# Performance work log

Hardware: AMD Instinct MI355X
Metric: run time of the kernel (lower is better)

## Reference

```python
import jax, jax.numpy as jnp
import numpy as np

HEADS, KV_HEADS, HEAD_DIM = 32, 8, 64


def apply_rope(x, cos, sin):
    # x: [b,h,s,d], cos/sin: [s, d//2]; pairs are interleaved (even/odd)
    c = cos[None, None, :, :]
    s = sin[None, None, :, :]
    x1 = x[..., 0::2]
    x2 = x[..., 1::2]
    xn = x1 * c - x2 * s
    yn = x1 * s + x2 * c
    return jnp.stack([xn, yn], axis=-1).reshape(x.shape)


def setup_inputs() -> dict:
    key = jax.random.key(0)
    ks = jax.random.split(key, 7)
    b, s, h = 1, 2048, 2048
    return {
        "x": jax.random.normal(ks[0], (b, s, h), jnp.float32),
        "cos": jax.random.normal(ks[1], (s, HEAD_DIM // 2), jnp.float32),
        "sin": jax.random.normal(ks[2], (s, HEAD_DIM // 2), jnp.float32),
        "Wq": jax.random.normal(ks[3], (h, HEADS * HEAD_DIM), jnp.float32) * 0.02,
        "Wk": jax.random.normal(ks[4], (h, KV_HEADS * HEAD_DIM), jnp.float32) * 0.02,
        "Wv": jax.random.normal(ks[5], (h, KV_HEADS * HEAD_DIM), jnp.float32) * 0.02,
        "Wo": jax.random.normal(ks[6], (HEADS * HEAD_DIM, h), jnp.float32) * 0.02,
    }


def reference(x, cos, sin, Wq, Wk, Wv, Wo):
    b, seq, hidden = x.shape
    Q = x @ Wq  # [b,s,H*d]
    K = x @ Wk  # [b,s,Kh*d]
    V = x @ Wv
    q = Q.reshape(b, seq, HEADS, HEAD_DIM).transpose(0, 2, 1, 3)      # b h s d
    k = K.reshape(b, seq, KV_HEADS, HEAD_DIM).transpose(0, 2, 1, 3)   # b k s d
    v = V.reshape(b, seq, KV_HEADS, HEAD_DIM).transpose(0, 2, 1, 3)
    r = HEADS // KV_HEADS
    # einops 'b k s d -> b (r k) s d': tile kv-head block r times
    k = jnp.tile(k, (1, r, 1, 1))
    v = jnp.tile(v, (1, r, 1, 1))
    q = apply_rope(q, cos, sin)
    k = apply_rope(k, cos, sin)
    scale = 1.0 / jnp.sqrt(jnp.float32(HEAD_DIM))
    qk = jnp.einsum('bhqd,bhkd->bhqk', q, k) * scale
    mask = jnp.triu(jnp.full((seq, seq), -jnp.inf, qk.dtype), k=1)
    attn = jax.nn.softmax(qk + mask, axis=-1)
    av = jnp.einsum('bhqk,bhkd->bhqd', attn, v)
    av = av.transpose(0, 2, 1, 3).reshape(b, seq, HEADS * HEAD_DIM)
    return av @ Wo
```

## Files before the change

kernel.cpp:

```cpp
#include <hip/hip_runtime.h>

typedef unsigned short u16;
typedef __attribute__((ext_vector_type(4))) float f32x4;
typedef __attribute__((ext_vector_type(16))) float f32x16;
typedef __attribute__((ext_vector_type(8))) __bf16 bf16x8;
typedef __attribute__((ext_vector_type(2))) __bf16 bf16x2;

#define HEADS 32
#define KV_HEADS 8
#define HD 64
#define SEQ 2048
#define HID 2048
#define NQK 3072
#define QSCALE (0.125f * 1.4426950408889634f)
#define OCH 2097152u

#define AS1 __attribute__((address_space(1)))
#define AS3 __attribute__((address_space(3)))

__device__ __forceinline__ u16 f2bf(float f) {
  unsigned u = __float_as_uint(f);
  u += 0x7FFFu + ((u >> 16) & 1u);
  return (u16)(u >> 16);
}

__device__ __forceinline__ unsigned pk2(float a, float b) {
  union { bf16x2 h; unsigned u; } c;
  c.h[0] = (__bf16)a; c.h[1] = (__bf16)b;
  return c.u;
}

__device__ __forceinline__ float bflo(unsigned u) {
  return __uint_as_float(u << 16);
}
__device__ __forceinline__ float bfhi(unsigned u) {
  return __uint_as_float(u & 0xFFFF0000u);
}

__device__ __forceinline__ void load16_to_lds(const void* g, void* l) {
  __builtin_amdgcn_global_load_lds((AS1 void*)(void*)g, (AS3 void*)l, 16, 0, 0);
}

__global__ __launch_bounds__(256) void k_f2b(const float* __restrict__ in,
                                             u16* __restrict__ out, int n4) {
  int i = blockIdx.x * 256 + threadIdx.x;
  if (i >= n4) return;
  float4 v = ((const float4*)in)[i];
  ushort4 o;
  o.x = f2bf(v.x); o.y = f2bf(v.y); o.z = f2bf(v.z); o.w = f2bf(v.w);
  ((ushort4*)out)[i] = o;
}

__global__ __launch_bounds__(256) void k_tconv4(const float* __restrict__ Wq,
                                                const float* __restrict__ Wk,
                                                const float* __restrict__ Wv,
                                                const float* __restrict__ Wo,
                                                u16* __restrict__ Wqkv,
                                                u16* __restrict__ WoT) {
  __shared__ float tile[32][33];
  int bid = blockIdx.x;
  const float* in; u16* out; int ldi, cx, cy;
  if (bid < 4096) {
    in = Wq; out = Wqkv; ldi = 2048; cx = bid & 63; cy = bid >> 6;
  } else if (bid < 5120) {
    int b = bid - 4096;
    in = Wk; out = Wqkv + (size_t)2048 * 2048; ldi = 512; cx = b & 15; cy = b >> 4;
  } else if (bid < 6144) {
    int b = bid - 5120;
    in = Wv; out = Wqkv + (size_t)2560 * 2048; ldi = 512; cx = b & 15; cy = b >> 4;
  } else {
    int b = bid - 6144;
    in = Wo; out = WoT; ldi = 2048; cx = b & 63; cy = b >> 6;
  }
  const int ldo = 2048;
  int c0 = cx * 32, r0 = cy * 32;
  int col = threadIdx.x & 31, rw = threadIdx.x >> 5;
#pragma unroll
  for (int i = 0; i < 4; i++)
    tile[rw + i * 8][col] = in[(size_t)(r0 + rw + i * 8) * ldi + c0 + col];
  __syncthreads();
#pragma unroll
  for (int i = 0; i < 4; i++)
    out[(size_t)(c0 + rw + i * 8) * ldo + r0 + col] = f2bf(tile[col][rw + i * 8]);
}


__device__ __forceinline__ void stage8(const u16* Ap, const u16* Bp, u16* AsX,
                                       u16* BsX, int tid, int K, int koff) {
#pragma unroll
  for (int i = 0; i < 4; i++) {
    load16_to_lds(Ap + (size_t)(i * 32) * K + koff, AsX + (i * 256 + tid) * 8);
    load16_to_lds(Bp + (size_t)(i * 32) * K + koff, BsX + (i * 256 + tid) * 8);
  }
}

__device__ __forceinline__ void frag16(const u16* Asb, const u16* Bsb,
                                       const int aoff[4][2], const int boff[4][2],
                                       f32x4 acc[4][4]) {
#pragma unroll
  for (int kk = 0; kk < 2; kk++) {
    bf16x8 a[4], b[4];
#pragma unroll
    for (int i = 0; i < 4; i++)
      a[i] = *(const bf16x8*)((const char*)Asb + aoff[i][kk]);
#pragma unroll
    for (int j = 0; j < 4; j++)
      b[j] = *(const bf16x8*)((const char*)Bsb + boff[j][kk]);
#pragma unroll
    for (int i = 0; i < 4; i++)
#pragma unroll
      for (int j = 0; j < 4; j++)
        acc[i][j] = __builtin_amdgcn_mfma_f32_16x16x32_bf16(a[i], b[j], acc[i][j], 0, 0, 0);
  }
}

#define TILE_STEP(AsX, BsX, tnext)                              \
  do {                                                          \
    asm volatile("s_waitcnt vmcnt(8)" ::: "memory");            \
    __builtin_amdgcn_sched_barrier(0);                          \
    __builtin_amdgcn_s_barrier();                               \
    frag16(AsX, BsX, aoff, boff, acc);                          \
    __builtin_amdgcn_sched_barrier(0);                          \
    __builtin_amdgcn_s_barrier();                               \
    stage8(Ap, Bp, AsX, BsX, tid, K, (tnext) * 64);             \
    __builtin_amdgcn_sched_barrier(0);                          \
  } while (0)

#define TILE_TAIL(AsX, BsX, n)                                  \
  do {                                                          \
    asm volatile("s_waitcnt vmcnt(" #n ")" ::: "memory");       \
    __builtin_amdgcn_sched_barrier(0);                          \
    __builtin_amdgcn_s_barrier();                               \
    frag16(AsX, BsX, aoff, boff, acc);                          \
  } while (0)

__global__ __launch_bounds__(256) void k_gemm(const u16* __restrict__ A,
                                              const u16* __restrict__ Bt,
                                              float* __restrict__ C,
                                              int M, int N, int K) {
  __shared__ u16 smem[32768];
  u16* As0 = smem;          u16* As1 = smem + 8192;
  u16* Bs0 = smem + 16384;  u16* Bs1 = smem + 24576;
  int tid = threadIdx.x;
  int m0 = blockIdx.x * 128, n0 = blockIdx.y * 128;
  int l = tid & 63, w = tid >> 6;
  int lr = l & 15, lg = l >> 4;
  int wr = (w >> 1) * 64, wc = (w & 1) * 64;
  f32x4 acc[4][4] = {};
  int r8 = tid >> 3;
  int sx = (tid & 7) ^ (r8 & 7);
  const u16* Ap = A + (size_t)(m0 + r8) * K + sx * 8;
  const u16* Bp = Bt + (size_t)(n0 + r8) * K + sx * 8;
  int aoff[4][2], boff[4][2];
#pragma unroll
  for (int i = 0; i < 4; i++) {
    int ra = wr + i * 16 + lr;
    int rb = wc + i * 16 + lr;
#pragma unroll
    for (int kk = 0; kk < 2; kk++) {
      aoff[i][kk] = ra * 128 + (((lg + kk * 4) ^ (ra & 7)) << 4);
      boff[i][kk] = rb * 128 + (((lg + kk * 4) ^ (rb & 7)) << 4);
    }
  }
  stage8(Ap, Bp, As0, Bs0, tid, K, 0);
  stage8(Ap, Bp, As1, Bs1, tid, K, 64);
#pragma unroll 1
  for (int t = 0; t < 30; t += 2) {
    TILE_STEP(As0, Bs0, t + 2);
    TILE_STEP(As1, Bs1, t + 3);
  }
  TILE_TAIL(As0, Bs0, 8);
  TILE_TAIL(As1, Bs1, 0);

#pragma unroll
  for (int i = 0; i < 4; i++)
#pragma unroll
    for (int j = 0; j < 4; j++)
#pragma unroll
      for (int r = 0; r < 4; r++)
        C[(size_t)(m0 + wr + i * 16 + lg * 4 + r) * N + n0 + wc + j * 16 + lr] =
            acc[i][j][r];
}


__device__ __forceinline__ void stageQ(const u16* Ap, const u16* Bp, u16* S,
                                       int tid, int koff) {
#pragma unroll
  for (int i = 0; i < 2; i++)
    load16_to_lds(Ap + (size_t)(i * 32) * HID + koff, S + (i * 256 + tid) * 8);
#pragma unroll
  for (int i = 0; i < 6; i++)
    load16_to_lds(Bp + (size_t)(i * 32) * HID + koff, S + 4096 + (i * 256 + tid) * 8);
}

__device__ __forceinline__ void frag26(const u16* Sb, const int aoff[2][2],
                                       const int boff[6][2], f32x4 acc[2][6]) {
#pragma unroll
  for (int kk = 0; kk < 2; kk++) {
    bf16x8 a[2], b[6];
#pragma unroll
    for (int i = 0; i < 2; i++)
      a[i] = *(const bf16x8*)((const char*)Sb + aoff[i][kk]);
#pragma unroll
    for (int j = 0; j < 6; j++)
      b[j] = *(const bf16x8*)((const char*)Sb + 8192 + boff[j][kk]);
    __builtin_amdgcn_s_setprio(1);
#pragma unroll
    for (int i = 0; i < 2; i++)
#pragma unroll
      for (int j = 0; j < 6; j++)
        acc[i][j] = __builtin_amdgcn_mfma_f32_16x16x32_bf16(a[i], b[j], acc[i][j], 0, 0, 0);
    __builtin_amdgcn_s_setprio(0);
  }
}

#define QK_STEP(Sc, tnext)                                      \
  do {                                                          \
    asm volatile("s_waitcnt vmcnt(8)" ::: "memory");            \
    __builtin_amdgcn_sched_barrier(0);                          \
    __builtin_amdgcn_s_barrier();                               \
    frag26(Sc, aoff, boff, acc);                                \
    __builtin_amdgcn_sched_barrier(0);                          \
    __builtin_amdgcn_s_barrier();                               \
    stageQ(Ap, Bp, Sc, tid, (tnext) * 64);                      \
    __builtin_amdgcn_sched_barrier(0);                          \
  } while (0)

#define QK_TAIL(Sc, n)                                          \
  do {                                                          \
    asm volatile("s_waitcnt vmcnt(" #n ")" ::: "memory");       \
    __builtin_amdgcn_sched_barrier(0);                          \
    __builtin_amdgcn_s_barrier();                               \
    frag26(Sc, aoff, boff, acc);                                \
  } while (0)

__global__ __launch_bounds__(256) void k_gemm_qkv(const u16* __restrict__ A,
                                                  const u16* __restrict__ Bt,
                                                  const float* __restrict__ cosp,
                                                  const float* __restrict__ sinp,
                                                  u16* __restrict__ qbuf,
                                                  u16* __restrict__ kbuf,
                                                  u16* __restrict__ vtb) {
  __shared__ u16 smem[32768];
  u16* S0 = smem;
  u16* S1 = smem + 16384;
  u16* Ts = smem;
  int tid = threadIdx.x;
  int bid = blockIdx.x;
  int wg = (bid & 7) * 64 + (bid >> 3);
  int m0 = (wg & 31) * 64, n0 = (wg >> 5) * 192;
  int l = tid & 63, w = tid >> 6;
  int lr = l & 15, lg = l >> 4;
  int wr = (w >> 1) * 32, wc = (w & 1) * 96;
  f32x4 acc[2][6] = {};
  int r8 = tid >> 3;
  int sx = (tid & 7) ^ (r8 & 7);
  const u16* Ap = A + (size_t)(m0 + r8) * HID + sx * 8;
  const u16* Bp = Bt + (size_t)(n0 + r8) * HID + sx * 8;
  int aoff[2][2], boff[6][2];
#pragma unroll
  for (int i = 0; i < 2; i++) {
    int ra = wr + i * 16 + lr;
#pragma unroll
    for (int kk = 0; kk < 2; kk++)
      aoff[i][kk] = ra * 128 + (((lg + kk * 4) ^ (ra & 7)) << 4);
  }
#pragma unroll
  for (int j = 0; j < 6; j++) {
    int rb = wc + j * 16 + lr;
#pragma unroll
    for (int kk = 0; kk < 2; kk++)
      boff[j][kk] = rb * 128 + (((lg + kk * 4) ^ (rb & 7)) << 4);
  }

  stageQ(Ap, Bp, S0, tid, 0);
  stageQ(Ap, Bp, S1, tid, 64);
#pragma unroll 1
  for (int t = 0; t < 30; t += 2) {
    QK_STEP(S0, t + 2);
    QK_STEP(S1, t + 3);
  }
  QK_TAIL(S0, 8);
  QK_TAIL(S1, 0);

  int odd = lr & 1;
#pragma unroll
  for (int j = 0; j < 6; j++) {
    int colf = n0 + wc + j * 16;
    if (colf < 2560) {
      bool isQ = colf < 2048;
      float scale = isQ ? QSCALE : 1.0f;
      u16* base = isQ ? qbuf + (size_t)(colf >> 6) * SEQ * HD
                      : kbuf + (size_t)((colf - 2048) >> 6) * SEQ * HD;
      int ch = colf & 63;
      int ii = (ch >> 1) + (lr >> 1);
#pragma unroll
      for (int i = 0; i < 2; i++)
#pragma unroll
        for (int r = 0; r < 4; r++) {
          float v = acc[i][j][r];
          float vp = __shfl_xor(v, 1, 64);
          int sr = m0 + wr + i * 16 + lg * 4 + r;
          float cs = cosp[sr * 32 + ii], sn = sinp[sr * 32 + ii];
          float x1 = odd ? vp : v, x2 = odd ? v : vp;
          float o = odd ? (x1 * sn + x2 * cs) : (x1 * cs - x2 * sn);
          base[(size_t)sr * HD + ch + lr] = f2bf(o * scale);
        }
    }
  }
  if (n0 + 192 > 2560) {
    __syncthreads();
#pragma unroll
    for (int j = 0; j < 6; j++) {
      int colf = n0 + wc + j * 16;
      if (colf >= 2560) {
#pragma unroll
        for (int i = 0; i < 2; i++)
#pragma unroll
          for (int r = 0; r < 4; r++) {
            int cB = wc + j * 16 + lr, rB = wr + i * 16 + lg * 4 + r;
            *(u16*)((char*)Ts + cB * 128 + ((rB * 2) ^ ((cB & 7) << 4))) =
                f2bf(acc[i][j][r]);
          }
      }
    }
    __syncthreads();
    int half = tid & 1;
#pragma unroll
    for (int p = 0; p < 2; p++) {
      int c = p * 128 + (tid >> 1);
      if (c < 192 && n0 + c >= 2560) {
        int col = n0 + c;
        int kvh = (col - 2560) >> 6, d = col & 63;
        u16* dst = vtb + (size_t)kvh * HD * SEQ + (size_t)d * SEQ + m0 + half * 32;
        const char* src = (const char*)Ts + c * 128;
        int cs7 = (c & 7) << 4;
#pragma unroll
        for (int q = 0; q < 4; q++)
          *(uint4*)(dst + q * 8) = *(const uint4*)(src + ((half * 64 + q * 16) ^ cs7));
      }
    }
  }
}

__global__ __launch_bounds__(256) void k_flash2(const u16* __restrict__ qb,
                                                const u16* __restrict__ kb,
                                                const u16* __restrict__ vt,
                                                unsigned* __restrict__ Opart,
                                                float2* __restrict__ ml) {
  __shared__ u16 Ks[2][64 * 64];
  __shared__ u16 Vs[2][64 * 64];
  int bid = blockIdx.x;
  int c = bid & 1;
  int b5 = bid >> 1;
  int h = b5 & 31;
  int qi = b5 >> 5;
  int qblk = (SEQ / 128) - 1 - qi;
  int kvh = h & 7;
  int tid = threadIdx.x, w = tid >> 6, l = tid & 63;
  int lq = l & 31, hi = l >> 5;
  const u16* qh = qb + (size_t)h * SEQ * HD;
  const u16* kh = kb + (size_t)kvh * SEQ * HD;
  const u16* vh = vt + (size_t)kvh * HD * SEQ;
  int wq0 = qblk * 128 + w * 32;
  int qg = wq0 + lq;

  bf16x8 qf[4];
#pragma unroll
  for (int ds = 0; ds < 4; ds++)
    qf[ds] = *(const bf16x8*)(qh + (size_t)qg * HD + ds * 16 + hi * 8);

  f32x16 acc[2] = {};
  float m_r = -__builtin_inff(), l_r = 0.f;

  int srow = tid >> 2, c4 = tid & 3, swz = (srow & 7) << 4;
  int sd0 = srow * 128 + ((c4 * 32) ^ swz);
  int sd1 = srow * 128 + ((c4 * 32 + 16) ^ swz);
  const int kt0 = c * (qblk + 1), kt1 = kt0 + qblk + 1;

  {
    const u16* ksrc = kh + (size_t)(kt0 * 64 + srow) * HD + c4 * 16;
    const u16* vsrc = vh + (size_t)srow * SEQ + kt0 * 64 + c4 * 16;
    uint4 a0 = *(const uint4*)(ksrc), a1 = *(const uint4*)(ksrc + 8);
    uint4 b0 = *(const uint4*)(vsrc), b1 = *(const uint4*)(vsrc + 8);
    *(uint4*)((char*)Ks[0] + sd0) = a0; *(uint4*)((char*)Ks[0] + sd1) = a1;
    *(uint4*)((char*)Vs[0] + sd0) = b0; *(uint4*)((char*)Vs[0] + sd1) = b1;
  }
  __syncthreads();

  uint4 kr0, kr1, vr0, vr1;
  int lswz = (lq & 7) << 4;
  for (int kt = kt0; kt < kt1; kt++) {
    int b = (kt - kt0) & 1;
    if (kt + 1 < kt1) {
      const u16* ksrc = kh + (size_t)((kt + 1) * 64 + srow) * HD + c4 * 16;
      const u16* vsrc = vh + (size_t)srow * SEQ + (kt + 1) * 64 + c4 * 16;
      kr0 = *(const uint4*)(ksrc); kr1 = *(const uint4*)(ksrc + 8);
      vr0 = *(const uint4*)(vsrc); vr1 = *(const uint4*)(vsrc + 8);
    }

    if (kt * 64 <= wq0 + 31) {
      f32x16 sT[2] = {};
      const char* kbase = (const char*)Ks[b];
      __builtin_amdgcn_s_setprio(1);
#pragma unroll
      for (int t = 0; t < 2; t++) {
#pragma unroll
        for (int ds = 0; ds < 4; ds++) {
          bf16x8 kf = *(const bf16x8*)(kbase + (t * 32 + lq) * 128 +
                                       ((ds * 32 + hi * 16) ^ lswz));
          sT[t] = __builtin_amdgcn_mfma_f32_32x32x16_bf16(kf, qf[ds], sT[t], 0, 0, 0);
        }
      }
      __builtin_amdgcn_s_setprio(0);

      if (kt * 64 + 63 > wq0) {
#pragma unroll
        for (int t = 0; t < 2; t++)
#pragma unroll
          for (int r = 0; r < 16; r++) {
            int kg = kt * 64 + t * 32 + (r & 3) + 8 * (r >> 2) + 4 * hi;
            if (kg > qg) sT[t][r] = -__builtin_inff();
          }
      }

      float pmax = sT[0][0];
#pragma unroll
      for (int r = 1; r < 16; r++) pmax = fmaxf(pmax, sT[0][r]);
#pragma unroll
      for (int r = 0; r < 16; r++) pmax = fmaxf(pmax, sT[1][r]);
      pmax = fmaxf(pmax, __shfl_xor(pmax, 32, 64));

      if (!__all(pmax <= m_r + 8.f)) {
        float mn = fmaxf(m_r, pmax);
        float scl = __builtin_amdgcn_exp2f(m_r - mn);
        l_r *= scl;
        acc[0] *= scl;
        acc[1] *= scl;
        m_r = mn;
      }

      float ss = 0.f;
#pragma unroll
      for (int t = 0; t < 2; t++)
#pragma unroll
        for (int r = 0; r < 16; r++) {
          float p = __builtin_amdgcn_exp2f(sT[t][r] - m_r);
          sT[t][r] = p;
          ss += p;
        }
      ss += __shfl_xor(ss, 32, 64);
      l_r += ss;

      const char* vbase = (const char*)Vs[b];
#pragma unroll
      for (int t = 0; t < 2; t++) {
        unsigned cp[4][2];
#pragma unroll
        for (int m = 0; m < 4; m++) {
          cp[m][0] = pk2(sT[t][4 * m + 0], sT[t][4 * m + 1]);
          cp[m][1] = pk2(sT[t][4 * m + 2], sT[t][4 * m + 3]);
        }
#pragma unroll
        for (int kl = 0; kl < 2; kl++) {
          unsigned s0 = hi ? cp[2 * kl][0] : cp[2 * kl + 1][0];
          unsigned s1 = hi ? cp[2 * kl][1] : cp[2 * kl + 1][1];
          unsigned r0 = (unsigned)__shfl_xor((int)s0, 32, 64);
          unsigned r1 = (unsigned)__shfl_xor((int)s1, 32, 64);
          union { unsigned u[4]; bf16x8 v; } pa;
          pa.u[0] = hi ? r0 : cp[2 * kl][0];
          pa.u[1] = hi ? r1 : cp[2 * kl][1];
          pa.u[2] = hi ? cp[2 * kl + 1][0] : r0;
          pa.u[3] = hi ? cp[2 * kl + 1][1] : r1;
          int ks = t * 2 + kl;
          __builtin_amdgcn_s_setprio(1);
#pragma unroll
          for (int dt = 0; dt < 2; dt++) {
            bf16x8 vb = *(const bf16x8*)(vbase + (dt * 32 + lq) * 128 +
                                         ((ks * 32 + hi * 16) ^ lswz));
            acc[dt] = __builtin_amdgcn_mfma_f32_32x32x16_bf16(vb, pa.v, acc[dt], 0, 0, 0);
          }
          __builtin_amdgcn_s_setprio(0);
        }
      }
    }

    if (kt + 1 < kt1) {
      *(uint4*)((char*)Ks[b ^ 1] + sd0) = kr0;
      *(uint4*)((char*)Ks[b ^ 1] + sd1) = kr1;
      *(uint4*)((char*)Vs[b ^ 1] + sd0) = vr0;
      *(uint4*)((char*)Vs[b ^ 1] + sd1) = vr1;
    }
    __syncthreads();
  }

  unsigned* op = Opart + (size_t)c * OCH + ((size_t)(b5 * 4 + w) * 16) * 64;
#pragma unroll
  for (int dt = 0; dt < 2; dt++)
#pragma unroll
    for (int j = 0; j < 8; j++)
      op[(dt * 8 + j) * 64 + l] = pk2(acc[dt][2 * j], acc[dt][2 * j + 1]);
  if (!hi)
    ml[c * (HEADS * SEQ) + h * SEQ + wq0 + lq] = make_float2(m_r, l_r);
}

__global__ __launch_bounds__(256) void k_merge(const unsigned* __restrict__ Opart,
                                               const float2* __restrict__ ml,
                                               u16* __restrict__ av) {
  __shared__ u16 Ts[8192];
  int bid = blockIdx.x;
  int h = bid & 31, qblk = bid >> 5;
  int b5 = ((SEQ / 128 - 1 - qblk) << 5) | h;
  int tid = threadIdx.x, w = tid >> 6, l = tid & 63;
  int lq = l & 31, hi = l >> 5;
  int wq0 = qblk * 128 + w * 32;

  float2 ml0 = ml[h * SEQ + wq0 + lq];
  float2 ml1 = ml[HEADS * SEQ + h * SEQ + wq0 + lq];
  float m = fmaxf(ml0.x, ml1.x);
  float f0 = __builtin_amdgcn_exp2f(ml0.x - m);
  float f1 = __builtin_amdgcn_exp2f(ml1.x - m);
  float inv = 1.0f / (ml0.y * f0 + ml1.y * f1);

  const unsigned* op0 = Opart + ((size_t)(b5 * 4 + w) * 16) * 64;
  const unsigned* op1 = op0 + OCH;
  f32x16 acc[2];
#pragma unroll
  for (int dt = 0; dt < 2; dt++)
#pragma unroll
    for (int j = 0; j < 8; j++) {
      unsigned a0 = op0[(dt * 8 + j) * 64 + l];
      unsigned a1 = op1[(dt * 8 + j) * 64 + l];
      acc[dt][2 * j] = bflo(a0) * f0 + bflo(a1) * f1;
      acc[dt][2 * j + 1] = bfhi(a0) * f0 + bfhi(a1) * f1;
    }

  int lswz = (lq & 7) << 4;
  char* wbase = (char*)Ts + w * 4096;
#pragma unroll
  for (int dt = 0; dt < 2; dt++)
#pragma unroll
    for (int m4 = 0; m4 < 4; m4++) {
      int r0 = 4 * m4;
      uint2 pr;
      pr.x = pk2(acc[dt][r0 + 0] * inv, acc[dt][r0 + 1] * inv);
      pr.y = pk2(acc[dt][r0 + 2] * inv, acc[dt][r0 + 3] * inv);
      int byte = lq * 128 + ((dt * 64 + m4 * 16 + hi * 8) ^ lswz);
      *(uint2*)(wbase + byte) = pr;
    }
  __syncthreads();
  int q2 = l >> 1, cH = l & 1;
  int qswz = (q2 & 7) << 4;
#pragma unroll
  for (int i = 0; i < 4; i++) {
    uint4 d = *(const uint4*)(wbase + q2 * 128 + ((cH * 64 + i * 16) ^ qswz));
    *(uint4*)(av + (size_t)(wq0 + q2) * HID + h * HD + cH * 32 + i * 8) = d;
  }
}

extern "C" void kernel_launch(void* const* d_in, const int* in_sizes, int n_in,
                              void* d_out, int out_size, void* d_ws, size_t ws_size,
                              hipStream_t stream) {
  (void)in_sizes; (void)n_in; (void)out_size; (void)ws_size;
  const float* x = (const float*)d_in[0];
  const float* cosp = (const float*)d_in[1];
  const float* sinp = (const float*)d_in[2];
  const float* Wq = (const float*)d_in[3];
  const float* Wk = (const float*)d_in[4];
  const float* Wv = (const float*)d_in[5];
  const float* Wo = (const float*)d_in[6];
  float* out = (float*)d_out;
  char* ws = (char*)d_ws;

  u16* xb = (u16*)(ws);
  float2* mlb = (float2*)(ws);
  u16* Wqkv = (u16*)(ws + ((size_t)8 << 20));
  u16* WoT = (u16*)(ws + ((size_t)20 << 20));
  u16* qbuf = (u16*)(ws + ((size_t)28 << 20));
  u16* kbuf = (u16*)(ws + ((size_t)36 << 20));
  u16* vtb = (u16*)(ws + ((size_t)38 << 20));
  u16* av = (u16*)(ws + ((size_t)40 << 20));
  unsigned* Opart = (unsigned*)(ws + ((size_t)48 << 20));

  k_f2b<<<(SEQ * HID / 4 + 255) / 256, 256, 0, stream>>>(x, xb, SEQ * HID / 4);
  k_tconv4<<<10240, 256, 0, stream>>>(Wq, Wk, Wv, Wo, Wqkv, WoT);
  k_gemm_qkv<<<512, 256, 0, stream>>>(xb, Wqkv, cosp, sinp, qbuf, kbuf, vtb);
  k_flash2<<<(SEQ / 128) * HEADS * 2, 256, 0, stream>>>(qbuf, kbuf, vtb, Opart, mlb);
  k_merge<<<(SEQ / 128) * HEADS, 256, 0, stream>>>(Opart, mlb, av);
  k_gemm<<<dim3(SEQ / 128, HID / 128), 256, 0, stream>>>(av, WoT, out, SEQ, HID, HID);
}
```

Baseline: 118.4 us.

## Drop split-KV flash attention and merge kernel; fuse input conversion kernels

Attention moves from a two-way split over the key range (1024 blocks writing bf16 partials plus max/sum, then a separate merge kernel) to a single pass per query block (512 blocks) that normalizes and writes the output directly, reusing the K shared buffer for the transpose. The x conversion kernel and the weight transpose/convert kernel are also merged into one launch. This removes two launches and the partial-output round trip through memory. In exchange each attention block does twice as many key tiles, giving less parallelism and a longer tail for the heaviest causal blocks.

```diff
diff --git a/kernel.cpp b/kernel.cpp
--- a/kernel.cpp
+++ b/kernel.cpp
@@ -13,7 +13,6 @@
 #define HID 2048
 #define NQK 3072
 #define QSCALE (0.125f * 1.4426950408889634f)
-#define OCH 2097152u
 
 #define AS1 __attribute__((address_space(1)))
 #define AS3 __attribute__((address_space(3)))
@@ -30,46 +29,40 @@
   return c.u;
 }
 
-__device__ __forceinline__ float bflo(unsigned u) {
-  return __uint_as_float(u << 16);
-}
-__device__ __forceinline__ float bfhi(unsigned u) {
-  return __uint_as_float(u & 0xFFFF0000u);
-}
-
 __device__ __forceinline__ void load16_to_lds(const void* g, void* l) {
   __builtin_amdgcn_global_load_lds((AS1 void*)(void*)g, (AS3 void*)l, 16, 0, 0);
 }
 
-__global__ __launch_bounds__(256) void k_f2b(const float* __restrict__ in,
-                                             u16* __restrict__ out, int n4) {
-  int i = blockIdx.x * 256 + threadIdx.x;
-  if (i >= n4) return;
-  float4 v = ((const float4*)in)[i];
-  ushort4 o;
-  o.x = f2bf(v.x); o.y = f2bf(v.y); o.z = f2bf(v.z); o.w = f2bf(v.w);
-  ((ushort4*)out)[i] = o;
-}
-
-__global__ __launch_bounds__(256) void k_tconv4(const float* __restrict__ Wq,
-                                                const float* __restrict__ Wk,
-                                                const float* __restrict__ Wv,
-                                                const float* __restrict__ Wo,
-                                                u16* __restrict__ Wqkv,
-                                                u16* __restrict__ WoT) {
+__global__ __launch_bounds__(256) void k_prep(const float* __restrict__ x,
+                                              const float* __restrict__ Wq,
+                                              const float* __restrict__ Wk,
+                                              const float* __restrict__ Wv,
+                                              const float* __restrict__ Wo,
+                                              u16* __restrict__ xb,
+                                              u16* __restrict__ Wqkv,
+                                              u16* __restrict__ WoT) {
   __shared__ float tile[32][33];
   int bid = blockIdx.x;
+  if (bid < 4096) {
+    int i = bid * 256 + threadIdx.x;
+    float4 v = ((const float4*)x)[i];
+    ushort4 o;
+    o.x = f2bf(v.x); o.y = f2bf(v.y); o.z = f2bf(v.z); o.w = f2bf(v.w);
+    ((ushort4*)xb)[i] = o;
+    return;
+  }
   const float* in; u16* out; int ldi, cx, cy;
-  if (bid < 4096) {
-    in = Wq; out = Wqkv; ldi = 2048; cx = bid & 63; cy = bid >> 6;
-  } else if (bid < 5120) {
+  if (bid < 8192) {
     int b = bid - 4096;
+    in = Wq; out = Wqkv; ldi = 2048; cx = b & 63; cy = b >> 6;
+  } else if (bid < 9216) {
+    int b = bid - 8192;
     in = Wk; out = Wqkv + (size_t)2048 * 2048; ldi = 512; cx = b & 15; cy = b >> 4;
-  } else if (bid < 6144) {
-    int b = bid - 5120;
+  } else if (bid < 10240) {
+    int b = bid - 9216;
     in = Wv; out = Wqkv + (size_t)2560 * 2048; ldi = 512; cx = b & 15; cy = b >> 4;
   } else {
-    int b = bid - 6144;
+    int b = bid - 10240;
     in = Wo; out = WoT; ldi = 2048; cx = b & 63; cy = b >> 6;
   }
   const int ldo = 2048;
@@ -343,19 +336,15 @@
   }
 }
 
-__global__ __launch_bounds__(256) void k_flash2(const u16* __restrict__ qb,
+__global__ __launch_bounds__(256) void k_flash1(const u16* __restrict__ qb,
                                                 const u16* __restrict__ kb,
                                                 const u16* __restrict__ vt,
-                                                unsigned* __restrict__ Opart,
-                                                float2* __restrict__ ml) {
+                                                u16* __restrict__ av) {
   __shared__ u16 Ks[2][64 * 64];
   __shared__ u16 Vs[2][64 * 64];
   int bid = blockIdx.x;
-  int c = bid & 1;
-  int b5 = bid >> 1;
-  int h = b5 & 31;
-  int qi = b5 >> 5;
-  int qblk = (SEQ / 128) - 1 - qi;
+  int h = bid & 31;
+  int qblk = (SEQ / 128) - 1 - (bid >> 5);
   int kvh = h & 7;
   int tid = threadIdx.x, w = tid >> 6, l = tid & 63;
   int lq = l & 31, hi = l >> 5;
@@ -376,11 +365,11 @@
   int srow = tid >> 2, c4 = tid & 3, swz = (srow & 7) << 4;
   int sd0 = srow * 128 + ((c4 * 32) ^ swz);
   int sd1 = srow * 128 + ((c4 * 32 + 16) ^ swz);
-  const int kt0 = c * (qblk + 1), kt1 = kt0 + qblk + 1;
+  const int nt = 2 * qblk + 2;
 
   {
-    const u16* ksrc = kh + (size_t)(kt0 * 64 + srow) * HD + c4 * 16;
-    const u16* vsrc = vh + (size_t)srow * SEQ + kt0 * 64 + c4 * 16;
+    const u16* ksrc = kh + (size_t)srow * HD + c4 * 16;
+    const u16* vsrc = vh + (size_t)srow * SEQ + c4 * 16;
     uint4 a0 = *(const uint4*)(ksrc), a1 = *(const uint4*)(ksrc + 8);
     uint4 b0 = *(const uint4*)(vsrc), b1 = *(const uint4*)(vsrc + 8);
     *(uint4*)((char*)Ks[0] + sd0) = a0; *(uint4*)((char*)Ks[0] + sd1) = a1;
@@ -390,9 +379,9 @@
 
   uint4 kr0, kr1, vr0, vr1;
   int lswz = (lq & 7) << 4;
-  for (int kt = kt0; kt < kt1; kt++) {
-    int b = (kt - kt0) & 1;
-    if (kt + 1 < kt1) {
+  for (int kt = 0; kt < nt; kt++) {
+    int b = kt & 1;
+    if (kt + 1 < nt) {
       const u16* ksrc = kh + (size_t)((kt + 1) * 64 + srow) * HD + c4 * 16;
       const u16* vsrc = vh + (size_t)srow * SEQ + (kt + 1) * 64 + c4 * 16;
       kr0 = *(const uint4*)(ksrc); kr1 = *(const uint4*)(ksrc + 8);
@@ -485,7 +474,7 @@
       }
     }
 
-    if (kt + 1 < kt1) {
+    if (kt + 1 < nt) {
       *(uint4*)((char*)Ks[b ^ 1] + sd0) = kr0;
       *(uint4*)((char*)Ks[b ^ 1] + sd1) = kr1;
       *(uint4*)((char*)Vs[b ^ 1] + sd0) = vr0;
@@ -494,49 +483,8 @@
     __syncthreads();
   }
 
-  unsigned* op = Opart + (size_t)c * OCH + ((size_t)(b5 * 4 + w) * 16) * 64;
-#pragma unroll
-  for (int dt = 0; dt < 2; dt++)
-#pragma unroll
-    for (int j = 0; j < 8; j++)
-      op[(dt * 8 + j) * 64 + l] = pk2(acc[dt][2 * j], acc[dt][2 * j + 1]);
-  if (!hi)
-    ml[c * (HEADS * SEQ) + h * SEQ + wq0 + lq] = make_float2(m_r, l_r);
-}
-
-__global__ __launch_bounds__(256) void k_merge(const unsigned* __restrict__ Opart,
-                                               const float2* __restrict__ ml,
-                                               u16* __restrict__ av) {
-  __shared__ u16 Ts[8192];
-  int bid = blockIdx.x;
-  int h = bid & 31, qblk = bid >> 5;
-  int b5 = ((SEQ / 128 - 1 - qblk) << 5) | h;
-  int tid = threadIdx.x, w = tid >> 6, l = tid & 63;
-  int lq = l & 31, hi = l >> 5;
-  int wq0 = qblk * 128 + w * 32;
-
-  float2 ml0 = ml[h * SEQ + wq0 + lq];
-  float2 ml1 = ml[HEADS * SEQ + h * SEQ + wq0 + lq];
-  float m = fmaxf(ml0.x, ml1.x);
-  float f0 = __builtin_amdgcn_exp2f(ml0.x - m);
-  float f1 = __builtin_amdgcn_exp2f(ml1.x - m);
-  float inv = 1.0f / (ml0.y * f0 + ml1.y * f1);
-
-  const unsigned* op0 = Opart + ((size_t)(b5 * 4 + w) * 16) * 64;
-  const unsigned* op1 = op0 + OCH;
-  f32x16 acc[2];
-#pragma unroll
-  for (int dt = 0; dt < 2; dt++)
-#pragma unroll
-    for (int j = 0; j < 8; j++) {
-      unsigned a0 = op0[(dt * 8 + j) * 64 + l];
-      unsigned a1 = op1[(dt * 8 + j) * 64 + l];
-      acc[dt][2 * j] = bflo(a0) * f0 + bflo(a1) * f1;
-      acc[dt][2 * j + 1] = bfhi(a0) * f0 + bfhi(a1) * f1;
-    }
-
-  int lswz = (lq & 7) << 4;
-  char* wbase = (char*)Ts + w * 4096;
+  float inv = 1.0f / l_r;
+  char* wbase = (char*)Ks[0] + w * 4096;
 #pragma unroll
   for (int dt = 0; dt < 2; dt++)
 #pragma unroll
@@ -573,19 +521,15 @@
   char* ws = (char*)d_ws;
 
   u16* xb = (u16*)(ws);
-  float2* mlb = (float2*)(ws);
   u16* Wqkv = (u16*)(ws + ((size_t)8 << 20));
   u16* WoT = (u16*)(ws + ((size_t)20 << 20));
   u16* qbuf = (u16*)(ws + ((size_t)28 << 20));
   u16* kbuf = (u16*)(ws + ((size_t)36 << 20));
   u16* vtb = (u16*)(ws + ((size_t)38 << 20));
   u16* av = (u16*)(ws + ((size_t)40 << 20));
-  unsigned* Opart = (unsigned*)(ws + ((size_t)48 << 20));
-
-  k_f2b<<<(SEQ * HID / 4 + 255) / 256, 256, 0, stream>>>(x, xb, SEQ * HID / 4);
-  k_tconv4<<<10240, 256, 0, stream>>>(Wq, Wk, Wv, Wo, Wqkv, WoT);
+
+  k_prep<<<14336, 256, 0, stream>>>(x, Wq, Wk, Wv, Wo, xb, Wqkv, WoT);
   k_gemm_qkv<<<512, 256, 0, stream>>>(xb, Wqkv, cosp, sinp, qbuf, kbuf, vtb);
-  k_flash2<<<(SEQ / 128) * HEADS * 2, 256, 0, stream>>>(qbuf, kbuf, vtb, Opart, mlb);
-  k_merge<<<(SEQ / 128) * HEADS, 256, 0, stream>>>(Opart, mlb, av);
+  k_flash1<<<512, 256, 0, stream>>>(qbuf, kbuf, vtb, av);
   k_gemm<<<dim3(SEQ / 128, HID / 128), 256, 0, stream>>>(av, WoT, out, SEQ, HID, HID);
 }
```

After: 131.3 us. +11.0%, slower.

## Split flash attention KV range four ways and fuse input conversion kernels

Applied to the files above, without the earlier changes.

The flash attention kernel now splits each query block's causal KV range into four chunks instead of two. This doubles the block count and evens out per-block work across the causal triangle. The merge kernel combines four partial outputs with their max and sum statistics. The x-to-bf16 conversion is folded into the weight transpose/convert kernel, removing one launch. The trade-off is more partial-output traffic and merge work, plus a reshuffled workspace layout that reuses dead buffers for the extra partials.

```diff
diff --git a/kernel.cpp b/kernel.cpp
--- a/kernel.cpp
+++ b/kernel.cpp
@@ -41,35 +41,36 @@
   __builtin_amdgcn_global_load_lds((AS1 void*)(void*)g, (AS3 void*)l, 16, 0, 0);
 }
 
-__global__ __launch_bounds__(256) void k_f2b(const float* __restrict__ in,
-                                             u16* __restrict__ out, int n4) {
-  int i = blockIdx.x * 256 + threadIdx.x;
-  if (i >= n4) return;
-  float4 v = ((const float4*)in)[i];
-  ushort4 o;
-  o.x = f2bf(v.x); o.y = f2bf(v.y); o.z = f2bf(v.z); o.w = f2bf(v.w);
-  ((ushort4*)out)[i] = o;
-}
-
-__global__ __launch_bounds__(256) void k_tconv4(const float* __restrict__ Wq,
-                                                const float* __restrict__ Wk,
-                                                const float* __restrict__ Wv,
-                                                const float* __restrict__ Wo,
-                                                u16* __restrict__ Wqkv,
-                                                u16* __restrict__ WoT) {
+__global__ __launch_bounds__(256) void k_prep(const float* __restrict__ x,
+                                              const float* __restrict__ Wq,
+                                              const float* __restrict__ Wk,
+                                              const float* __restrict__ Wv,
+                                              const float* __restrict__ Wo,
+                                              u16* __restrict__ xb,
+                                              u16* __restrict__ Wqkv,
+                                              u16* __restrict__ WoT) {
   __shared__ float tile[32][33];
   int bid = blockIdx.x;
+  if (bid < 4096) {
+    int i = bid * 256 + threadIdx.x;
+    float4 v = ((const float4*)x)[i];
+    ushort4 o;
+    o.x = f2bf(v.x); o.y = f2bf(v.y); o.z = f2bf(v.z); o.w = f2bf(v.w);
+    ((ushort4*)xb)[i] = o;
+    return;
+  }
   const float* in; u16* out; int ldi, cx, cy;
-  if (bid < 4096) {
-    in = Wq; out = Wqkv; ldi = 2048; cx = bid & 63; cy = bid >> 6;
-  } else if (bid < 5120) {
+  if (bid < 8192) {
     int b = bid - 4096;
+    in = Wq; out = Wqkv; ldi = 2048; cx = b & 63; cy = b >> 6;
+  } else if (bid < 9216) {
+    int b = bid - 8192;
     in = Wk; out = Wqkv + (size_t)2048 * 2048; ldi = 512; cx = b & 15; cy = b >> 4;
-  } else if (bid < 6144) {
-    int b = bid - 5120;
+  } else if (bid < 10240) {
+    int b = bid - 9216;
     in = Wv; out = Wqkv + (size_t)2560 * 2048; ldi = 512; cx = b & 15; cy = b >> 4;
   } else {
-    int b = bid - 6144;
+    int b = bid - 10240;
     in = Wo; out = WoT; ldi = 2048; cx = b & 63; cy = b >> 6;
   }
   const int ldo = 2048;
@@ -83,7 +84,6 @@
   for (int i = 0; i < 4; i++)
     out[(size_t)(c0 + rw + i * 8) * ldo + r0 + col] = f2bf(tile[col][rw + i * 8]);
 }
-
 
 __device__ __forceinline__ void stage8(const u16* Ap, const u16* Bp, u16* AsX,
                                        u16* BsX, int tid, int K, int koff) {
@@ -181,7 +181,6 @@
         C[(size_t)(m0 + wr + i * 16 + lg * 4 + r) * N + n0 + wc + j * 16 + lr] =
             acc[i][j][r];
 }
-
 
 __device__ __forceinline__ void stageQ(const u16* Ap, const u16* Bp, u16* S,
                                        int tid, int koff) {
@@ -346,13 +345,14 @@
 __global__ __launch_bounds__(256) void k_flash2(const u16* __restrict__ qb,
                                                 const u16* __restrict__ kb,
                                                 const u16* __restrict__ vt,
-                                                unsigned* __restrict__ Opart,
+                                                unsigned* __restrict__ OpA,
+                                                unsigned* __restrict__ OpB,
                                                 float2* __restrict__ ml) {
   __shared__ u16 Ks[2][64 * 64];
   __shared__ u16 Vs[2][64 * 64];
   int bid = blockIdx.x;
-  int c = bid & 1;
-  int b5 = bid >> 1;
+  int c = bid & 3;
+  int b5 = bid >> 2;
   int h = b5 & 31;
   int qi = b5 >> 5;
   int qblk = (SEQ / 128) - 1 - qi;
@@ -376,7 +376,8 @@
   int srow = tid >> 2, c4 = tid & 3, swz = (srow & 7) << 4;
   int sd0 = srow * 128 + ((c4 * 32) ^ swz);
   int sd1 = srow * 128 + ((c4 * 32 + 16) ^ swz);
-  const int kt0 = c * (qblk + 1), kt1 = kt0 + qblk + 1;
+  const int nt = 2 * qblk + 2;
+  const int kt0 = (c * nt) >> 2, kt1 = ((c + 1) * nt) >> 2;
 
   {
     const u16* ksrc = kh + (size_t)(kt0 * 64 + srow) * HD + c4 * 16;
@@ -494,7 +495,8 @@
     __syncthreads();
   }
 
-  unsigned* op = Opart + (size_t)c * OCH + ((size_t)(b5 * 4 + w) * 16) * 64;
+  unsigned* op = (c < 2 ? OpA + (size_t)c * OCH : OpB + (size_t)(c - 2) * OCH) +
+                 ((size_t)(b5 * 4 + w) * 16) * 64;
 #pragma unroll
   for (int dt = 0; dt < 2; dt++)
 #pragma unroll
@@ -504,7 +506,8 @@
     ml[c * (HEADS * SEQ) + h * SEQ + wq0 + lq] = make_float2(m_r, l_r);
 }
 
-__global__ __launch_bounds__(256) void k_merge(const unsigned* __restrict__ Opart,
+__global__ __launch_bounds__(256) void k_merge(const unsigned* __restrict__ OpA,
+                                               const unsigned* __restrict__ OpB,
                                                const float2* __restrict__ ml,
                                                u16* __restrict__ av) {
   __shared__ u16 Ts[8192];
@@ -515,24 +518,37 @@
   int lq = l & 31, hi = l >> 5;
   int wq0 = qblk * 128 + w * 32;
 
-  float2 ml0 = ml[h * SEQ + wq0 + lq];
-  float2 ml1 = ml[HEADS * SEQ + h * SEQ + wq0 + lq];
-  float m = fmaxf(ml0.x, ml1.x);
-  float f0 = __builtin_amdgcn_exp2f(ml0.x - m);
-  float f1 = __builtin_amdgcn_exp2f(ml1.x - m);
-  float inv = 1.0f / (ml0.y * f0 + ml1.y * f1);
-
-  const unsigned* op0 = Opart + ((size_t)(b5 * 4 + w) * 16) * 64;
-  const unsigned* op1 = op0 + OCH;
+  float2 mlv[4];
+#pragma unroll
+  for (int cc = 0; cc < 4; cc++)
+    mlv[cc] = ml[cc * (HEADS * SEQ) + h * SEQ + wq0 + lq];
+  float m = fmaxf(fmaxf(mlv[0].x, mlv[1].x), fmaxf(mlv[2].x, mlv[3].x));
+  float f[4], denom = 0.f;
+#pragma unroll
+  for (int cc = 0; cc < 4; cc++) {
+    f[cc] = __builtin_amdgcn_exp2f(mlv[cc].x - m);
+    denom += mlv[cc].y * f[cc];
+  }
+  float inv = 1.0f / denom;
+
+  size_t wo = ((size_t)(b5 * 4 + w) * 16) * 64;
+  const unsigned* op[4];
+  op[0] = OpA + wo; op[1] = OpA + OCH + wo;
+  op[2] = OpB + wo; op[3] = OpB + OCH + wo;
+
   f32x16 acc[2];
 #pragma unroll
   for (int dt = 0; dt < 2; dt++)
 #pragma unroll
     for (int j = 0; j < 8; j++) {
-      unsigned a0 = op0[(dt * 8 + j) * 64 + l];
-      unsigned a1 = op1[(dt * 8 + j) * 64 + l];
-      acc[dt][2 * j] = bflo(a0) * f0 + bflo(a1) * f1;
-      acc[dt][2 * j + 1] = bfhi(a0) * f0 + bfhi(a1) * f1;
+      unsigned a0 = op[0][(dt * 8 + j) * 64 + l];
+      unsigned a1 = op[1][(dt * 8 + j) * 64 + l];
+      unsigned a2 = op[2][(dt * 8 + j) * 64 + l];
+      unsigned a3 = op[3][(dt * 8 + j) * 64 + l];
+      acc[dt][2 * j] = bflo(a0) * f[0] + bflo(a1) * f[1] +
+                       bflo(a2) * f[2] + bflo(a3) * f[3];
+      acc[dt][2 * j + 1] = bfhi(a0) * f[0] + bfhi(a1) * f[1] +
+                           bfhi(a2) * f[2] + bfhi(a3) * f[3];
     }
 
   int lswz = (lq & 7) << 4;
@@ -573,19 +589,19 @@
   char* ws = (char*)d_ws;
 
   u16* xb = (u16*)(ws);
-  float2* mlb = (float2*)(ws);
   u16* Wqkv = (u16*)(ws + ((size_t)8 << 20));
   u16* WoT = (u16*)(ws + ((size_t)20 << 20));
   u16* qbuf = (u16*)(ws + ((size_t)28 << 20));
   u16* kbuf = (u16*)(ws + ((size_t)36 << 20));
   u16* vtb = (u16*)(ws + ((size_t)38 << 20));
   u16* av = (u16*)(ws + ((size_t)40 << 20));
-  unsigned* Opart = (unsigned*)(ws + ((size_t)48 << 20));
-
-  k_f2b<<<(SEQ * HID / 4 + 255) / 256, 256, 0, stream>>>(x, xb, SEQ * HID / 4);
-  k_tconv4<<<10240, 256, 0, stream>>>(Wq, Wk, Wv, Wo, Wqkv, WoT);
+  unsigned* OpA = (unsigned*)(ws + ((size_t)48 << 20));
+  unsigned* OpB = (unsigned*)(ws);
+  float2* mlb = (float2*)(ws + ((size_t)16 << 20));
+
+  k_prep<<<14336, 256, 0, stream>>>(x, Wq, Wk, Wv, Wo, xb, Wqkv, WoT);
   k_gemm_qkv<<<512, 256, 0, stream>>>(xb, Wqkv, cosp, sinp, qbuf, kbuf, vtb);
-  k_flash2<<<(SEQ / 128) * HEADS * 2, 256, 0, stream>>>(qbuf, kbuf, vtb, Opart, mlb);
-  k_merge<<<(SEQ / 128) * HEADS, 256, 0, stream>>>(Opart, mlb, av);
+  k_flash2<<<2048, 256, 0, stream>>>(qbuf, kbuf, vtb, OpA, OpB, mlb);
+  k_merge<<<512, 256, 0, stream>>>(OpA, OpB, mlb, av);
   k_gemm<<<dim3(SEQ / 128, HID / 128), 256, 0, stream>>>(av, WoT, out, SEQ, HID, HID);
 }
```

After: 120.9 us. 2.1% more time.
